# Kernel tuning notes

Hardware: AMD Instinct MI355X
Metric: run time of the kernel (lower is better)

## Reference

```python
import jax, jax.numpy as jnp
import numpy as np

B, T, NI, NH, NO = 32, 2048, 1, 512, 1


def setup_inputs() -> dict:
    key = jax.random.key(0)
    ks = jax.random.split(key, 7)
    x = jax.random.normal(ks[0], (B, T, NI), dtype=jnp.float32)
    # torch code draws h_0 ~ U[-1,1) once and tiles over batch; here per-batch uniform
    h_0 = jax.random.uniform(ks[1], (B, NH), dtype=jnp.float32) * 2.0 - 1.0
    w_input_std = 1.0 / np.sqrt(NH)
    W_ih = jax.random.normal(ks[2], (NH, NI), dtype=jnp.float32) * w_input_std
    prob_c = 0.1
    w_hidden_std = 1.5 / np.sqrt(prob_c * NH)
    mask = jax.random.bernoulli(ks[3], prob_c, (NH, NH)).astype(jnp.float32)
    W_hh = jax.random.normal(ks[4], (NH, NH), dtype=jnp.float32) * w_hidden_std * mask
    W_hz = jax.random.normal(ks[5], (NO, NH), dtype=jnp.float32) * w_input_std
    W_zh = jax.random.uniform(ks[6], (NH, NO), dtype=jnp.float32, minval=-1.0, maxval=1.0)
    return {"x": x, "h_0": h_0, "W_ih": W_ih, "W_hh": W_hh, "W_hz": W_hz, "W_zh": W_zh}


def reference(x, h_0, W_ih, W_hh, W_hz, W_zh):
    dt, tau = 0.001, 0.01
    alpha = dt / tau  # 0.1
    # precompute input projection for all timesteps: [T, B, NH]
    x_proj = jnp.einsum('bti,hi->tbh', x, W_ih)

    def step(carry, xp_t):
        h_prev, z_prev = carry  # [B,NH], [B,NO]
        h_transfer = jnp.tanh(h_prev)
        dhdt = -h_prev + h_transfer @ W_hh.T + xp_t + z_prev @ W_zh.T
        h_t = h_prev + alpha * dhdt
        z_t = jnp.tanh(h_t) @ W_hz.T
        return (h_t, z_t), (h_t, z_t)

    z0 = jnp.tanh(h_0) @ W_hz.T
    _, (h, z) = jax.lax.scan(step, (h_0, z0), x_proj)
    # scan stacks time first -> [T,B,*]; transpose to [B,T,*]
    return jnp.swapaxes(z, 0, 1), jnp.swapaxes(h, 0, 1)
```

## Files before the change

### kernel.cpp

```cpp
#include <hip/hip_runtime.h>


#define NH   512
#define TT   2048
#define BB   32
#define PAD  96
#define PIN  80
#define NONE_ 0xFF

__global__ __launch_bounds__(512) void count_nnz(
    const float* __restrict__ Whh, int* __restrict__ nnz) {
  const int wib  = threadIdx.x >> 6;
  const int lane = threadIdx.x & 63;
  const int row  = blockIdx.x * 8 + wib;
  const float* wrow = Whh + (size_t)row * NH;
  int cnt = 0;
  for (int c = 0; c < NH / 64; ++c)
    cnt += __popcll(__ballot(wrow[c * 64 + lane] != 0.0f));
  if (lane == 0) nnz[row] = cnt;
}

__global__ __launch_bounds__(512) void sort_rows(
    const int* __restrict__ nnz, int* __restrict__ perm) {
  __shared__ int nl[NH];
  const int j = threadIdx.x;
  const int my = nnz[j];
  nl[j] = my;
  __syncthreads();
  int r = 0;
  const int4* p4 = (const int4*)nl;
  for (int i = 0; i < NH / 4; ++i) {
    int4 v = p4[i];
    const int base = i * 4;
    r += (v.x > my) || (v.x == my && base + 0 < j);
    r += (v.y > my) || (v.y == my && base + 1 < j);
    r += (v.z > my) || (v.z == my && base + 2 < j);
    r += (v.w > my) || (v.w == my && base + 3 < j);
  }
  perm[r] = j;
}

__global__ __launch_bounds__(64) void build_color(
    const float* __restrict__ Whh, const int* __restrict__ perm,
    float* __restrict__ vals, unsigned* __restrict__ offs,
    int* __restrict__ cntw) {
  __shared__ unsigned short occ[64][32];
  __shared__ unsigned char  mL[2][32][PAD];
  __shared__ unsigned char  mB[2][32][PAD];
  __shared__ unsigned freeL[2][32][3];
  __shared__ unsigned freeB[2][32][3];
  __shared__ short pB[2][128], pL[2][128];
  __shared__ int cwsh;

  const int lane = threadIdx.x;
  const int g    = blockIdx.x;
  const int p    = g * 64 + lane;
  const int hl   = lane >> 5;
  const int li   = lane & 31;
  const int row  = perm[p];
  const float* wrow = Whh + (size_t)row * NH;

  if (lane == 0) cwsh = 0;
  for (int b = 0; b < 32; ++b) {
    unsigned m16 = 0;
    for (int m = 0; m < 16; ++m)
      m16 |= (wrow[b + 32 * m] != 0.f) ? (1u << m) : 0u;
    occ[lane][b] = (unsigned short)m16;
  }
  for (int c = 0; c < PAD; ++c) { mL[hl][li][c] = NONE_; mB[hl][li][c] = NONE_; }
  #pragma unroll
  for (int w2 = 0; w2 < 3; ++w2) {
    freeL[hl][li][w2] = 0xFFFFFFFFu;
    freeB[hl][li][w2] = 0xFFFFFFFFu;
  }
  __syncthreads();

  if (li == 0) {
    int maxc = 0;
    for (int l = 0; l < 32; ++l) {
      const int gl = hl * 32 + l;
      for (int b = 0; b < 32; ++b) {
        const int mult = __popc((unsigned)occ[gl][b]);
        for (int m = 0; m < mult; ++m) {
          int c = -1;
          #pragma unroll
          for (int w2 = 0; w2 < 3; ++w2) {
            unsigned cm = freeL[hl][l][w2] & freeB[hl][b][w2];
            if (cm) { c = w2 * 32 + __ffs(cm) - 1; break; }
          }
          if (c >= 0) {
            mL[hl][l][c] = (unsigned char)b;
            mB[hl][b][c] = (unsigned char)l;
            freeL[hl][l][c >> 5] &= ~(1u << (c & 31));
            freeB[hl][b][c >> 5] &= ~(1u << (c & 31));
            if (c > maxc) maxc = c;
            continue;
          }
          int a = -1, be = -1;
          #pragma unroll
          for (int w2 = 0; w2 < 3; ++w2) {
            unsigned mm = freeL[hl][l][w2];
            if (mm) { a = w2 * 32 + __ffs(mm) - 1; break; }
          }
          #pragma unroll
          for (int w2 = 0; w2 < 3; ++w2) {
            unsigned mm = freeB[hl][b][w2];
            if (mm) { be = w2 * 32 + __ffs(mm) - 1; break; }
          }
          if (a < 0) continue;
          if (be < 0) {
            mL[hl][l][a] = (unsigned char)b;
            freeL[hl][l][a >> 5] &= ~(1u << (a & 31));
            if (a > maxc) maxc = a;
            continue;
          }
          int n = 0, curN = b, curCol = a, isbank = 1, of = 0;
          for (;;) {
            int nxt = isbank ? (int)mB[hl][curN][curCol]
                             : (int)mL[hl][curN][curCol];
            if (nxt == NONE_) break;
            if (n >= 128) { of = 1; break; }
            pB[hl][n] = (short)(isbank ? curN : nxt);
            pL[hl][n] = (short)(isbank ? nxt : curN);
            ++n;
            curN = nxt; isbank ^= 1;
            curCol = (curCol == a) ? be : a;
          }
          if (of) {
            mL[hl][l][a] = (unsigned char)b;
            freeL[hl][l][a >> 5] &= ~(1u << (a & 31));
            if (a > maxc) maxc = a;
            continue;
          }
          for (int i = 0; i < n; ++i) {
            int oc = (i & 1) ? be : a;
            mB[hl][pB[hl][i]][oc] = NONE_;
            mL[hl][pL[hl][i]][oc] = NONE_;
          }
          for (int i = 0; i < n; ++i) {
            int nc = (i & 1) ? a : be;
            mB[hl][pB[hl][i]][nc] = (unsigned char)pL[hl][i];
            mL[hl][pL[hl][i]][nc] = (unsigned char)pB[hl][i];
          }
          freeB[hl][b][a >> 5]  ^= (1u << (a & 31));
          freeB[hl][b][be >> 5] ^= (1u << (be & 31));
          if (isbank) {
            freeB[hl][curN][a >> 5]  ^= (1u << (a & 31));
            freeB[hl][curN][be >> 5] ^= (1u << (be & 31));
          } else {
            freeL[hl][curN][a >> 5]  ^= (1u << (a & 31));
            freeL[hl][curN][be >> 5] ^= (1u << (be & 31));
          }
          mL[hl][l][a] = (unsigned char)b;
          mB[hl][b][a] = (unsigned char)l;
          freeL[hl][l][a >> 5] &= ~(1u << (a & 31));
          freeB[hl][b][a >> 5] &= ~(1u << (a & 31));
          if (a > maxc) maxc = a;
        }
      }
    }
    atomicMax(&cwsh, maxc + 1);
  }
  __syncthreads();

  for (int b = 0; b < 32; ++b) {
    int need = __popc((unsigned)occ[lane][b]);
    int have = 0;
    for (int c = 0; c < PAD; ++c) have += (mL[hl][li][c] == b);
    while (have < need) {
      for (int c = 0; c < PAD; ++c)
        if (mL[hl][li][c] == NONE_) {
          mL[hl][li][c] = (unsigned char)b;
          atomicMax(&cwsh, c + 1);
          break;
        }
      ++have;
    }
  }
  __syncthreads();
  if (lane == 0) cntw[g] = cwsh;

  for (int c = 0; c < PAD; ++c) {
    int b = mL[hl][li][c];
    float v = 0.f; unsigned col = 0u;
    if (b != NONE_) {
      unsigned m16 = (unsigned)occ[lane][b];
      int m = __ffs(m16) - 1;
      occ[lane][b] = (unsigned short)(m16 & (m16 - 1u));
      col = (unsigned)(b + 32 * m);
      v = wrow[col];
    }
    vals[c * NH + p] = v;
    offs[c * NH + p] = col;
  }
}

template <int CTRL, int RM>
__device__ __forceinline__ float dppadd(float v) {
  int t = __builtin_amdgcn_update_dpp(0, __float_as_int(v), CTRL, RM, 0xF, true);
  return v + __int_as_float(t);
}
__device__ __forceinline__ float wave_sum_lane63(float v) {
  v = dppadd<0xB1,  0xF>(v);
  v = dppadd<0x4E,  0xF>(v);
  v = dppadd<0x141, 0xF>(v);
  v = dppadd<0x140, 0xF>(v);
  v = dppadd<0x142, 0xA>(v);
  v = dppadd<0x143, 0xC>(v);
  return v;
}

__device__ __forceinline__ float ftanh(float x) {
  float xc = fminf(9.0f, fmaxf(-9.0f, x));
  float t  = __expf(2.0f * xc);
  return (t - 1.0f) * __builtin_amdgcn_rcpf(t + 1.0f);
}

#define GA(T_RD, E) (*(const float*)((const char*)(T_RD) + cidx[E]))

#define ESN_STEP(T_RD, T_WR, RWR, SIDX)                                      \
  {                                                                          \
    float d0 = 0.f, d1 = 0.f, d2 = 0.f, d3 = 0.f;                            \
    _Pragma("unroll")                                                        \
    for (int e = 0; e < PAD; e += 8) {                                       \
      if (e < cw) {                                                          \
        d0 = fmaf(wval[e + 0], GA(T_RD, e + 0), d0);                         \
        d1 = fmaf(wval[e + 1], GA(T_RD, e + 1), d1);                         \
        d2 = fmaf(wval[e + 2], GA(T_RD, e + 2), d2);                         \
        d3 = fmaf(wval[e + 3], GA(T_RD, e + 3), d3);                         \
        d0 = fmaf(wval[e + 4], GA(T_RD, e + 4), d0);                         \
        d1 = fmaf(wval[e + 5], GA(T_RD, e + 5), d1);                         \
        d2 = fmaf(wval[e + 6], GA(T_RD, e + 6), d2);                         \
        d3 = fmaf(wval[e + 7], GA(T_RD, e + 7), d3);                         \
      }                                                                      \
    }                                                                        \
    float dot  = (d0 + d1) + (d2 + d3);                                      \
    float xp   = x_lds[SIDX] * w_ih;                                         \
    float dhdt = ((dot - h) + xp) + z_prev * w_zh;                           \
    float hn   = h + 0.1f * dhdt;                                            \
    float thn  = ftanh(hn);                                                  \
    T_WR[row] = thn;                                                         \
    oh[(SIDX) * NH + row] = hn;                                              \
    float pzs = wave_sum_lane63(thn * w_hz);                                 \
    if (lane == 63) red[RWR][wid] = pzs;                                     \
    asm volatile("s_waitcnt lgkmcnt(0)\n\ts_barrier" ::: "memory");          \
    float4 r0 = *(const float4*)&red[RWR][0];                                \
    float4 r1 = *(const float4*)&red[RWR][4];                                \
    float z = ((r0.x + r0.y) + (r0.z + r0.w)) + ((r1.x + r1.y) + (r1.z + r1.w)); \
    if (p == 0) oz[SIDX] = z;                                                \
    z_prev = z; h = hn;                                                      \
  }

__global__ __launch_bounds__(512, 2) void esn_steps(
    const float* __restrict__ x,   const float* __restrict__ h0,
    const float* __restrict__ Wih, const float* __restrict__ Whz,
    const float* __restrict__ Wzh, const float* __restrict__ vals,
    const unsigned* __restrict__ offs, const int* __restrict__ perm,
    const int* __restrict__ cntw, float* __restrict__ out) {
  __shared__ float t_lds[2][NH];
  __shared__ float x_lds[TT];
  __shared__ __align__(16) float red[2][8];

  const int p    = threadIdx.x;
  const int b    = blockIdx.x;
  const int lane = p & 63;
  const int wid  = p >> 6;
  const int row  = perm[p];

  float* t0 = t_lds[0];
  float* t1 = t_lds[1];

  for (int i = p; i < TT; i += NH) x_lds[i] = x[(size_t)b * TT + i];

  int cw = __builtin_amdgcn_readfirstlane((cntw[wid] + 7) & ~7);

  float    wval[PAD];
  unsigned cidx[PAD];
  #pragma unroll
  for (int e = 0; e < PAD; ++e) {
    wval[e] = vals[e * NH + p];
    cidx[e] = offs[e * NH + p] * 4u;
  }
  #pragma unroll
  for (int e = 0; e < PIN; ++e)
    asm volatile("" : "+v"(wval[e]), "+v"(cidx[e]));

  const float w_ih = Wih[row];
  const float w_hz = Whz[row];
  const float w_zh = Wzh[row];
  float h = h0[(size_t)b * NH + row];

  float* oz = out + (size_t)b * TT;
  float* oh = out + (size_t)BB * TT + (size_t)b * TT * NH;

  float th0 = ftanh(h);
  t0[row] = th0;
  float pz = wave_sum_lane63(th0 * w_hz);
  if (lane == 63) red[0][wid] = pz;
  __syncthreads();
  float4 i0 = *(const float4*)&red[0][0];
  float4 i1 = *(const float4*)&red[0][4];
  float z_prev = ((i0.x + i0.y) + (i0.z + i0.w)) + ((i1.x + i1.y) + (i1.z + i1.w));

  for (int s = 0; s < TT; s += 2) {
    ESN_STEP(t0, t1, 1, s);
    ESN_STEP(t1, t0, 0, s + 1);
  }
}

extern "C" void kernel_launch(void* const* d_in, const int* in_sizes, int n_in,
                              void* d_out, int out_size, void* d_ws,
                              size_t ws_size, hipStream_t stream) {
  const float* x   = (const float*)d_in[0];
  const float* h0  = (const float*)d_in[1];
  const float* Wih = (const float*)d_in[2];
  const float* Whh = (const float*)d_in[3];
  const float* Whz = (const float*)d_in[4];
  const float* Wzh = (const float*)d_in[5];
  float* out = (float*)d_out;

  float*    vals = (float*)d_ws;
  unsigned* offs = (unsigned*)(vals + PAD * NH);
  int*      nnz  = (int*)(offs + PAD * NH);
  int*      perm = nnz + NH;
  int*      cntw = perm + NH;

  hipLaunchKernelGGL(count_nnz, dim3(NH / 8), dim3(512), 0, stream, Whh, nnz);
  hipLaunchKernelGGL(sort_rows, dim3(1), dim3(512), 0, stream, nnz, perm);
  hipLaunchKernelGGL(build_color, dim3(8), dim3(64), 0, stream,
                     Whh, perm, vals, offs, cntw);
  hipLaunchKernelGGL(esn_steps, dim3(BB), dim3(512), 0, stream,
                     x, h0, Wih, Whz, Wzh, vals, offs, perm, cntw, out);
}
```

Before: 3.196 ms.

## Replace bank-conflict edge coloring with greedy slot scheduling and finer padding

Swaps the bipartite edge-coloring schedule (with alternating-path recoloring) for a greedy assignment. Each nonzero takes the first slot that is free for both its row lane and its LDS bank, or failing that the first slot free for the lane. The per-step gather loop now pads the slot count to multiples of 4 instead of 8, and launch bounds drop to one block per SM with more register-pinned entries. This trims wasted padded FMAs and lets the compiler use more registers, at the cost of possibly more LDS bank conflicts and a longer schedule when the greedy pass fails to find a shared slot.

```diff
diff --git a/kernel.cpp b/kernel.cpp
--- a/kernel.cpp
+++ b/kernel.cpp
@@ -5,7 +5,7 @@
 #define TT   2048
 #define BB   32
 #define PAD  96
-#define PIN  80
+#define PIN  88
 #define NONE_ 0xFF
 
 __global__ __launch_bounds__(512) void count_nnz(
@@ -40,16 +40,14 @@
   perm[r] = j;
 }
 
-__global__ __launch_bounds__(64) void build_color(
+__global__ __launch_bounds__(64) void build_sched(
     const float* __restrict__ Whh, const int* __restrict__ perm,
     float* __restrict__ vals, unsigned* __restrict__ offs,
     int* __restrict__ cntw) {
   __shared__ unsigned short occ[64][32];
-  __shared__ unsigned char  mL[2][32][PAD];
-  __shared__ unsigned char  mB[2][32][PAD];
+  __shared__ unsigned char  sb[64][PAD];
   __shared__ unsigned freeL[2][32][3];
   __shared__ unsigned freeB[2][32][3];
-  __shared__ short pB[2][128], pL[2][128];
   __shared__ int cwsh;
 
   const int lane = threadIdx.x;
@@ -67,7 +65,7 @@
       m16 |= (wrow[b + 32 * m] != 0.f) ? (1u << m) : 0u;
     occ[lane][b] = (unsigned short)m16;
   }
-  for (int c = 0; c < PAD; ++c) { mL[hl][li][c] = NONE_; mB[hl][li][c] = NONE_; }
+  for (int c = 0; c < PAD; ++c) sb[lane][c] = NONE_;
   #pragma unroll
   for (int w2 = 0; w2 < 3; ++w2) {
     freeL[hl][li][w2] = 0xFFFFFFFFu;
@@ -88,100 +86,28 @@
             unsigned cm = freeL[hl][l][w2] & freeB[hl][b][w2];
             if (cm) { c = w2 * 32 + __ffs(cm) - 1; break; }
           }
-          if (c >= 0) {
-            mL[hl][l][c] = (unsigned char)b;
-            mB[hl][b][c] = (unsigned char)l;
-            freeL[hl][l][c >> 5] &= ~(1u << (c & 31));
-            freeB[hl][b][c >> 5] &= ~(1u << (c & 31));
-            if (c > maxc) maxc = c;
-            continue;
+          const bool common = (c >= 0);
+          if (!common) {
+            #pragma unroll
+            for (int w2 = 0; w2 < 3; ++w2) {
+              unsigned lm = freeL[hl][l][w2];
+              if (c < 0 && lm) c = w2 * 32 + __ffs(lm) - 1;
+            }
           }
-          int a = -1, be = -1;
-          #pragma unroll
-          for (int w2 = 0; w2 < 3; ++w2) {
-            unsigned mm = freeL[hl][l][w2];
-            if (mm) { a = w2 * 32 + __ffs(mm) - 1; break; }
-          }
-          #pragma unroll
-          for (int w2 = 0; w2 < 3; ++w2) {
-            unsigned mm = freeB[hl][b][w2];
-            if (mm) { be = w2 * 32 + __ffs(mm) - 1; break; }
-          }
-          if (a < 0) continue;
-          if (be < 0) {
-            mL[hl][l][a] = (unsigned char)b;
-            freeL[hl][l][a >> 5] &= ~(1u << (a & 31));
-            if (a > maxc) maxc = a;
-            continue;
-          }
-          int n = 0, curN = b, curCol = a, isbank = 1, of = 0;
-          for (;;) {
-            int nxt = isbank ? (int)mB[hl][curN][curCol]
-                             : (int)mL[hl][curN][curCol];
-            if (nxt == NONE_) break;
-            if (n >= 128) { of = 1; break; }
-            pB[hl][n] = (short)(isbank ? curN : nxt);
-            pL[hl][n] = (short)(isbank ? nxt : curN);
-            ++n;
-            curN = nxt; isbank ^= 1;
-            curCol = (curCol == a) ? be : a;
-          }
-          if (of) {
-            mL[hl][l][a] = (unsigned char)b;
-            freeL[hl][l][a >> 5] &= ~(1u << (a & 31));
-            if (a > maxc) maxc = a;
-            continue;
-          }
-          for (int i = 0; i < n; ++i) {
-            int oc = (i & 1) ? be : a;
-            mB[hl][pB[hl][i]][oc] = NONE_;
-            mL[hl][pL[hl][i]][oc] = NONE_;
-          }
-          for (int i = 0; i < n; ++i) {
-            int nc = (i & 1) ? a : be;
-            mB[hl][pB[hl][i]][nc] = (unsigned char)pL[hl][i];
-            mL[hl][pL[hl][i]][nc] = (unsigned char)pB[hl][i];
-          }
-          freeB[hl][b][a >> 5]  ^= (1u << (a & 31));
-          freeB[hl][b][be >> 5] ^= (1u << (be & 31));
-          if (isbank) {
-            freeB[hl][curN][a >> 5]  ^= (1u << (a & 31));
-            freeB[hl][curN][be >> 5] ^= (1u << (be & 31));
-          } else {
-            freeL[hl][curN][a >> 5]  ^= (1u << (a & 31));
-            freeL[hl][curN][be >> 5] ^= (1u << (be & 31));
-          }
-          mL[hl][l][a] = (unsigned char)b;
-          mB[hl][b][a] = (unsigned char)l;
-          freeL[hl][l][a >> 5] &= ~(1u << (a & 31));
-          freeB[hl][b][a >> 5] &= ~(1u << (a & 31));
-          if (a > maxc) maxc = a;
+          sb[gl][c] = (unsigned char)b;
+          freeL[hl][l][c >> 5] &= ~(1u << (c & 31));
+          if (common) freeB[hl][b][c >> 5] &= ~(1u << (c & 31));
+          if (c > maxc) maxc = c;
         }
       }
     }
     atomicMax(&cwsh, maxc + 1);
   }
   __syncthreads();
-
-  for (int b = 0; b < 32; ++b) {
-    int need = __popc((unsigned)occ[lane][b]);
-    int have = 0;
-    for (int c = 0; c < PAD; ++c) have += (mL[hl][li][c] == b);
-    while (have < need) {
-      for (int c = 0; c < PAD; ++c)
-        if (mL[hl][li][c] == NONE_) {
-          mL[hl][li][c] = (unsigned char)b;
-          atomicMax(&cwsh, c + 1);
-          break;
-        }
-      ++have;
-    }
-  }
-  __syncthreads();
   if (lane == 0) cntw[g] = cwsh;
 
   for (int c = 0; c < PAD; ++c) {
-    int b = mL[hl][li][c];
+    int b = sb[lane][c];
     float v = 0.f; unsigned col = 0u;
     if (b != NONE_) {
       unsigned m16 = (unsigned)occ[lane][b];
@@ -222,16 +148,12 @@
   {                                                                          \
     float d0 = 0.f, d1 = 0.f, d2 = 0.f, d3 = 0.f;                            \
     _Pragma("unroll")                                                        \
-    for (int e = 0; e < PAD; e += 8) {                                       \
+    for (int e = 0; e < PAD; e += 4) {                                       \
       if (e < cw) {                                                          \
         d0 = fmaf(wval[e + 0], GA(T_RD, e + 0), d0);                         \
         d1 = fmaf(wval[e + 1], GA(T_RD, e + 1), d1);                         \
         d2 = fmaf(wval[e + 2], GA(T_RD, e + 2), d2);                         \
         d3 = fmaf(wval[e + 3], GA(T_RD, e + 3), d3);                         \
-        d0 = fmaf(wval[e + 4], GA(T_RD, e + 4), d0);                         \
-        d1 = fmaf(wval[e + 5], GA(T_RD, e + 5), d1);                         \
-        d2 = fmaf(wval[e + 6], GA(T_RD, e + 6), d2);                         \
-        d3 = fmaf(wval[e + 7], GA(T_RD, e + 7), d3);                         \
       }                                                                      \
     }                                                                        \
     float dot  = (d0 + d1) + (d2 + d3);                                      \
@@ -251,7 +173,7 @@
     z_prev = z; h = hn;                                                      \
   }
 
-__global__ __launch_bounds__(512, 2) void esn_steps(
+__global__ __launch_bounds__(512, 1) void esn_steps(
     const float* __restrict__ x,   const float* __restrict__ h0,
     const float* __restrict__ Wih, const float* __restrict__ Whz,
     const float* __restrict__ Wzh, const float* __restrict__ vals,
@@ -272,7 +194,7 @@
 
   for (int i = p; i < TT; i += NH) x_lds[i] = x[(size_t)b * TT + i];
 
-  int cw = __builtin_amdgcn_readfirstlane((cntw[wid] + 7) & ~7);
+  int cw = __builtin_amdgcn_readfirstlane((cntw[wid] + 3) & ~3);
 
   float    wval[PAD];
   unsigned cidx[PAD];
@@ -327,7 +249,7 @@
 
   hipLaunchKernelGGL(count_nnz, dim3(NH / 8), dim3(512), 0, stream, Whh, nnz);
   hipLaunchKernelGGL(sort_rows, dim3(1), dim3(512), 0, stream, nnz, perm);
-  hipLaunchKernelGGL(build_color, dim3(8), dim3(64), 0, stream,
+  hipLaunchKernelGGL(build_sched, dim3(8), dim3(64), 0, stream,
                      Whh, perm, vals, offs, cntw);
   hipLaunchKernelGGL(esn_steps, dim3(BB), dim3(512), 0, stream,
                      x, h0, Wih, Whz, Wzh, vals, offs, perm, cntw, out);
```

Result: slower. 3.395 ms (+6.2%).
